# Kernel optimization log

Hardware: AMD Instinct MI355X
Metric: run time of the kernel (lower is better)

The kernel has to match this reference:

```python
import jax, jax.numpy as jnp
import numpy as np

ALPHA = 2.0  # spikingjelly default ATan surrogate alpha
EPS = 1e-5   # BatchNorm eps

@jax.custom_vjp
def heaviside_atan(x):
    return (x >= 0.0).astype(x.dtype)

def _ha_fwd(x):
    return heaviside_atan(x), x

def _ha_bwd(x, g):
    return (g * ALPHA / (2.0 * (1.0 + (jnp.pi / 2.0 * ALPHA * x) ** 2)),)

heaviside_atan.defvjp(_ha_fwd, _ha_bwd)

def lif(x_seq, tau=2.0, v_th=1.0):
    # MultiStepLIFNode, v_reset=0 (hard reset), detach_reset=True
    def step(v, x):
        v = v + (x - v) / tau
        s = heaviside_atan(v - v_th)
        v = v * (1.0 - jax.lax.stop_gradient(s))
        return v, s
    _, spikes = jax.lax.scan(step, jnp.zeros_like(x_seq[0]), x_seq)
    return spikes

def conv_bn(y, Wt, g, b):
    # 1x1 conv (no bias) + BatchNorm2d in training mode over flattened (T*B, H, W)
    y = jnp.einsum('tbchw,oc->tbohw', y, Wt)
    m = y.mean(axis=(0, 1, 3, 4), keepdims=True)
    v = y.var(axis=(0, 1, 3, 4), keepdims=True)
    C = Wt.shape[0]
    return (y - m) / jnp.sqrt(v + EPS) * g.reshape(1, 1, C, 1, 1) + b.reshape(1, 1, C, 1, 1)

def setup_inputs() -> dict:
    key = jax.random.key(0)
    ks = jax.random.split(key, 5)
    T, B, C, H, W = 4, 64, 384, 14, 14
    x = jax.random.normal(ks[0], (T, B, C, H, W), dtype=jnp.float32)
    Wq = jax.random.normal(ks[1], (C, C), dtype=jnp.float32) * 0.02
    Wk = jax.random.normal(ks[2], (C, C), dtype=jnp.float32) * 0.02
    Wv = jax.random.normal(ks[3], (C, C), dtype=jnp.float32) * 0.02
    Wp = jax.random.normal(ks[4], (C, C), dtype=jnp.float32) * 0.02
    ones = jnp.ones((C,), jnp.float32)
    zeros = jnp.zeros((C,), jnp.float32)
    return {"x": x, "Wq": Wq, "Wk": Wk, "Wv": Wv, "Wp": Wp,
            "gq": ones, "bq": zeros, "gk": ones, "bk": zeros,
            "gv": ones, "bv": zeros, "gp": ones, "bp": zeros}

def reference(x, Wq, Wk, Wv, Wp, gq, bq, gk, bk, gv, bv, gp, bp):
    T, B, C, H, W = x.shape
    nh = 8
    dh = C // nh
    N = H * W

    xs = lif(x)  # pre_lif

    def heads(y):  # [T,B,C,H,W] -> [T,B,h,N,dh]
        y = y.reshape(T, B, C, N).transpose(0, 1, 3, 2)
        return y.reshape(T, B, N, nh, dh).transpose(0, 1, 3, 2, 4)

    q = heads(lif(conv_bn(xs, Wq, gq, bq)))
    k = heads(lif(conv_bn(xs, Wk, gk, bk)))
    v = heads(lif(conv_bn(xs, Wv, gv, bv)))

    attn = jnp.einsum('tbhnd,tbhmd->tbhnm', q, k)      # no softmax
    o = jnp.einsum('tbhnm,tbhmd->tbhnd', attn, v) * 0.125
    o = o.transpose(0, 1, 2, 4, 3).reshape(T, B, C, N).reshape(T, B, C, H, W)
    o = lif(o, v_th=0.5)                                # attn_lif
    return conv_bn(o, Wp, gp, bp)                       # proj (no lif)
```

## Files before the change

### kernel.cpp

```cpp
#include <hip/hip_runtime.h>
#include <hip/hip_bf16.h>
#include <stdint.h>

#define T_  4
#define B_  64
#define C_  384
#define N_  196
#define NH  8
#define DH  48
#define TB_ (T_*B_)
#define R_  (T_*B_*N_)
#define NW  12
#define P_  12544
#define NCH 66
#define KG_ 17

typedef float f32x2 __attribute__((ext_vector_type(2)));

__global__ void transpose_w4(const float* __restrict__ s0, const float* __restrict__ s1,
                             const float* __restrict__ s2, const float* __restrict__ s3,
                             float* __restrict__ dst){
    int m = blockIdx.y;
    const float* src = (m==0)?s0:(m==1)?s1:(m==2)?s2:s3;
    int idx = blockIdx.x*256 + threadIdx.x;
    if (idx >= C_*C_) return;
    int o = idx % C_, c = idx / C_;
    dst[(size_t)m*C_*C_ + idx] = src[o*C_ + c];
}

__global__ __launch_bounds__(256) void pre_lif(const float* __restrict__ x,
                                               uint32_t* __restrict__ maskXS){
    int b = blockIdx.x / NW;
    int w = blockIdx.x % NW;
    int n = threadIdx.x;
    if (n >= N_) return;
    float v[32];
#pragma unroll
    for (int j=0;j<32;j++) v[j] = 0.f;
#pragma unroll
    for (int t=0;t<T_;t++){
        uint32_t word = 0;
#pragma unroll
        for (int j=0;j<32;j++){
            int c = w*32 + j;
            float xv = x[((size_t)(t*B_+b)*C_ + c)*N_ + n];
            v[j] = v[j] + (xv - v[j])*0.5f;
            if (v[j] >= 1.0f){ word |= (1u<<j); v[j] = 0.f; }
        }
        maskXS[((size_t)(t*B_+b)*N_ + n)*NW + w] = word;
    }
}

__global__ __launch_bounds__(256) void bit_transpose(const uint32_t* __restrict__ mask,
                                                     unsigned long long* __restrict__ maskT){
    int gw = blockIdx.x*4 + (threadIdx.x>>6);
    int lane = threadIdx.x & 63;
    int kc = gw/12, kw = gw%12;
    uint32_t mwv[12];
#pragma unroll
    for (int w=0;w<12;w++) mwv[w]=0u;
    if (gw < 784){
        int pix = gw*64 + lane;
        const uint4* m4 = (const uint4*)(mask + (size_t)pix*NW);
        uint4 a=m4[0], b=m4[1], c=m4[2];
        mwv[0]=a.x; mwv[1]=a.y; mwv[2]=a.z; mwv[3]=a.w;
        mwv[4]=b.x; mwv[5]=b.y; mwv[6]=b.z; mwv[7]=b.w;
        mwv[8]=c.x; mwv[9]=c.y; mwv[10]=c.z; mwv[11]=c.w;
    }
#pragma unroll
    for (int w=0; w<12; w++){
        uint32_t word = mwv[w];
#pragma unroll
        for (int j=0; j<32; j++){
            unsigned long long bal = __ballot((int)((word>>j)&1u));
            if (lane == 0)
                maskT[((size_t)kc*C_ + (w*32+j))*12 + kw] = bal;
        }
    }
}

__global__ __launch_bounds__(256) void gram(const unsigned long long* __restrict__ maskT,
                                            unsigned int* __restrict__ Gpart){
    __shared__ unsigned int tile[64][49];
    int tid = threadIdx.x, wave = tid>>6, lane = tid&63;
    int kg = blockIdx.x, rg = blockIdx.y, cg = blockIdx.z;
    for (int i=tid; i<64*49; i+=256) ((unsigned int*)tile)[i] = 0u;
    __syncthreads();
    int kc = kg*4 + wave;
    if (kc < NCH){
        const uint4* rp = (const uint4*)(maskT + ((size_t)kc*C_ + rg*64 + lane)*12);
        uint32_t row[24];
#pragma unroll
        for (int q=0;q<6;q++){
            uint4 a = rp[q];
            row[4*q]=a.x; row[4*q+1]=a.y; row[4*q+2]=a.z; row[4*q+3]=a.w;
        }
        for (int cc=0; cc<48; cc++){
            const uint4* cp = (const uint4*)(maskT + ((size_t)kc*C_ + cg*48 + cc)*12);
            uint32_t col[24];
#pragma unroll
            for (int q=0;q<6;q++){
                uint4 a = cp[q];
                col[4*q]=a.x; col[4*q+1]=a.y; col[4*q+2]=a.z; col[4*q+3]=a.w;
            }
            unsigned int s = 0;
#pragma unroll
            for (int q=0;q<24;q++) s += (unsigned int)__popc(row[q]&col[q]);
            atomicAdd(&tile[lane][cc], s);
        }
    }
    __syncthreads();
    unsigned int* out = Gpart + (size_t)kg*C_*C_;
    for (int i=tid; i<64*48; i+=256){
        int r = i/48, cc = i%48;
        out[(size_t)(rg*64+r)*C_ + cg*48 + cc] = tile[r][cc];
    }
}

__global__ __launch_bounds__(256) void gram_reduce(const unsigned int* __restrict__ Gpart,
                                                   float* __restrict__ Gf){
    int e = blockIdx.x*256 + threadIdx.x;
    unsigned int s = 0;
#pragma unroll
    for (int k=0;k<KG_;k++) s += Gpart[(size_t)k*C_*C_ + e];
    Gf[e] = (float)s;
}

__global__ __launch_bounds__(384) void bn_from_gram(const float* __restrict__ Gf,
        const float* __restrict__ WTall,
        const float* __restrict__ g0, const float* __restrict__ b0,
        const float* __restrict__ g1, const float* __restrict__ b1,
        const float* __restrict__ g2, const float* __restrict__ b2,
        float* __restrict__ scaleOut, float* __restrict__ shiftOut, int wtBase){
    __shared__ float w4[384][4];
    __shared__ float sred[8][6];
    int t = threadIdx.x, wave = t>>6, lane = t&63;
    int br = blockIdx.y;
    const float* WT = WTall + (size_t)(wtBase+br)*C_*C_;
    int o0 = blockIdx.x*4;
    float4 wv = *(const float4*)(WT + (size_t)t*C_ + o0);
    w4[t][0]=wv.x; w4[t][1]=wv.y; w4[t][2]=wv.z; w4[t][3]=wv.w;
    __syncthreads();
    float h0=0.f,h1=0.f,h2=0.f,h3=0.f;
#pragma unroll 4
    for (int c=0;c<C_;c++){
        float gv = Gf[(size_t)c*C_ + t];
        float4 wc = *(const float4*)&w4[c][0];
        h0 += gv*wc.x; h1 += gv*wc.y; h2 += gv*wc.z; h3 += gv*wc.w;
    }
    float cnt = Gf[(size_t)t*C_ + t];
    float p0=wv.x*h0, p1=wv.y*h1, p2=wv.z*h2, p3=wv.w*h3;
    float q0=cnt*wv.x, q1=cnt*wv.y, q2=cnt*wv.z, q3=cnt*wv.w;
#pragma unroll
    for (int off=32; off>0; off>>=1){
        p0+=__shfl_down(p0,off); p1+=__shfl_down(p1,off);
        p2+=__shfl_down(p2,off); p3+=__shfl_down(p3,off);
        q0+=__shfl_down(q0,off); q1+=__shfl_down(q1,off);
        q2+=__shfl_down(q2,off); q3+=__shfl_down(q3,off);
    }
    if (lane == 0){
        sred[0][wave]=p0; sred[1][wave]=p1; sred[2][wave]=p2; sred[3][wave]=p3;
        sred[4][wave]=q0; sred[5][wave]=q1; sred[6][wave]=q2; sred[7][wave]=q3;
    }
    __syncthreads();
    if (t < 4){
        const float* g  = (br==0)?g0:(br==1)?g1:g2;
        const float* bb = (br==0)?b0:(br==1)?b1:b2;
        float ss = ((sred[t][0]+sred[t][1])+(sred[t][2]+sred[t][3]))+(sred[t][4]+sred[t][5]);
        float sm = ((sred[4+t][0]+sred[4+t][1])+(sred[4+t][2]+sred[4+t][3]))+(sred[4+t][4]+sred[4+t][5]);
        float m   = sm / (float)R_;
        float var = ss / (float)R_ - m*m;
        float sc  = g[o0+t] / sqrtf(var + 1e-5f);
        scaleOut[br*C_ + o0+t] = sc;
        shiftOut[br*C_ + o0+t] = bb[o0+t] - m*sc;
    }
}

__global__ __launch_bounds__(256) void conv_lif3(const uint32_t* __restrict__ mask,
        const float* __restrict__ WTall,
        const float* __restrict__ scaleAll, const float* __restrict__ shiftAll,
        uint32_t* __restrict__ moQ, uint32_t* __restrict__ moK, uint32_t* __restrict__ moV){
    __shared__ uint16_t lst[4][416];
    __shared__ float scLDS[3*C_];
    __shared__ float shLDS[3*C_];
    int tid = threadIdx.x, wave = tid>>6, lane = tid&63;
    int pix0 = blockIdx.x*4 + wave;
    for (int i=tid; i<3*C_; i+=256){ scLDS[i]=scaleAll[i]; shLDS[i]=shiftAll[i]; }
    __syncthreads();

    float v0[6]={0,0,0,0,0,0}, v1[6]={0,0,0,0,0,0}, v2[6]={0,0,0,0,0,0};
    for (int t=0;t<T_;t++){
        size_t pix = (size_t)t*P_ + pix0;
        const uint4* m4 = (const uint4*)(mask + pix*NW);
        uint4 ma = m4[0], mb = m4[1], mc = m4[2];
        uint32_t mwv[12] = {ma.x,ma.y,ma.z,ma.w, mb.x,mb.y,mb.z,mb.w, mc.x,mc.y,mc.z,mc.w};
        int cnt = 0;
#pragma unroll
        for (int w=0;w<12;w++) cnt += __popc(mwv[w]);
        if (lane < 12){
            int off = 0;
            uint32_t mybits = 0;
#pragma unroll
            for (int w=0;w<12;w++){
                if (w < lane) off += __popc(mwv[w]);
                if (w == lane) mybits = mwv[w];
            }
            while (mybits){
                lst[wave][off++] = (uint16_t)((lane<<5) + __builtin_ctz(mybits));
                mybits &= mybits - 1;
            }
        }
        __syncthreads();

#pragma unroll
        for (int br=0; br<3; ++br){
            const float* WT = WTall + (size_t)br*C_*C_ + lane;
            float ya[6]={0,0,0,0,0,0}, yb[6]={0,0,0,0,0,0};
            float yc[6]={0,0,0,0,0,0}, yd[6]={0,0,0,0,0,0};
            int i = 0;
            for (; i+3 < cnt; i += 4){
                ushort4 cs = *(const ushort4*)&lst[wave][i];
                const float* q0 = WT + (size_t)cs.x*C_;
                const float* q1 = WT + (size_t)cs.y*C_;
                const float* q2 = WT + (size_t)cs.z*C_;
                const float* q3 = WT + (size_t)cs.w*C_;
#pragma unroll
                for (int j=0;j<6;j++){
                    ya[j] += q0[j<<6]; yb[j] += q1[j<<6];
                    yc[j] += q2[j<<6]; yd[j] += q3[j<<6];
                }
            }
            for (; i < cnt; ++i){
                int c = lst[wave][i];
                const float* q0 = WT + (size_t)c*C_;
#pragma unroll
                for (int j=0;j<6;j++) ya[j] += q0[j<<6];
            }
            float* vs = (br==0)?v0:(br==1)?v1:v2;
            uint32_t words[12];
#pragma unroll
            for (int j=0;j<6;j++){
                int o = (j<<6) + lane;
                float val = ((ya[j]+yb[j])+(yc[j]+yd[j]))*scLDS[br*C_+o] + shLDS[br*C_+o];
                float vv = vs[j];
                vv = vv + (val - vv)*0.5f;
                int s = (vv >= 1.0f);
                unsigned long long bal = __ballot(s);
                if (s) vv = 0.f;
                vs[j] = vv;
                words[2*j]   = (uint32_t)bal;
                words[2*j+1] = (uint32_t)(bal>>32);
            }
            if (lane == 0){
                uint32_t* mo = (br==0)?moQ:(br==1)?moK:moV;
                uint4* o4 = (uint4*)(mo + pix*NW);
                o4[0] = make_uint4(words[0],words[1],words[2],words[3]);
                o4[1] = make_uint4(words[4],words[5],words[6],words[7]);
                o4[2] = make_uint4(words[8],words[9],words[10],words[11]);
            }
        }
        __syncthreads();
    }
}

__global__ __launch_bounds__(256) void attention_lif(const uint32_t* __restrict__ mq,
                                                     const uint32_t* __restrict__ mk,
                                                     const uint32_t* __restrict__ mv,
                                                     uint16_t* __restrict__ mo){
    __shared__ unsigned long long kT[DH][4];
    __shared__ unsigned long long vT[DH][4];
    __shared__ uint32_t Cp[DH*25];

    int h = blockIdx.x & 7;
    int b = blockIdx.x >> 3;
    int tid = threadIdx.x, wv = tid>>6, lane = tid&63;
    int sw  = (h*DH) >> 5;
    int shf = (h*DH) & 31;

    float vm[DH];
#pragma unroll
    for (int d=0;d<DH;d++) vm[d] = 0.f;

    for (int t=0;t<T_;t++){
        int tb = t*B_ + b;
        unsigned long long q = 0, kk = 0, vvv = 0;
        if (tid < N_){
            const uint32_t* pq = mq + ((size_t)tb*N_ + tid)*NW + sw;
            const uint32_t* pk = mk + ((size_t)tb*N_ + tid)*NW + sw;
            const uint32_t* pv = mv + ((size_t)tb*N_ + tid)*NW + sw;
            unsigned long long lo, hi;
            lo = pq[0]; hi = pq[1];
            q   = (shf ? ((lo>>16) | (hi<<16)) : (lo | (hi<<32))) & 0xFFFFFFFFFFFFULL;
            lo = pk[0]; hi = pk[1];
            kk  = (shf ? ((lo>>16) | (hi<<16)) : (lo | (hi<<32))) & 0xFFFFFFFFFFFFULL;
            lo = pv[0]; hi = pv[1];
            vvv = (shf ? ((lo>>16) | (hi<<16)) : (lo | (hi<<32))) & 0xFFFFFFFFFFFFULL;
        }
#pragma unroll 1
        for (int d=0; d<DH; d++){
            unsigned long long bk_ = __ballot((int)((kk >>d)&1ull));
            unsigned long long bv_ = __ballot((int)((vvv>>d)&1ull));
            if (lane == 0){ kT[d][wv] = bk_; vT[d][wv] = bv_; }
        }
        __syncthreads();

        if (tid < 240){
            int j  = tid / 5;
            int dg = tid % 5;
            int d0 = dg*10;
            int d1 = (dg==4) ? 48 : d0+10;
            unsigned long long ka=kT[j][0], kb=kT[j][1], kc=kT[j][2], kd=kT[j][3];
            for (int d=d0; d<d1; d+=2){
                uint32_t c0 = (uint32_t)(__popcll(ka&vT[d][0]) + __popcll(kb&vT[d][1])
                            + __popcll(kc&vT[d][2]) + __popcll(kd&vT[d][3]));
                uint32_t c1 = (uint32_t)(__popcll(ka&vT[d+1][0]) + __popcll(kb&vT[d+1][1])
                            + __popcll(kc&vT[d+1][2]) + __popcll(kd&vT[d+1][3]));
                Cp[j*25 + (d>>1)] = c0 | (c1<<16);
            }
        }
        __syncthreads();

        if (tid < N_){
            uint32_t acc[24];
#pragma unroll
            for (int p=0;p<24;p++) acc[p] = 0u;
            unsigned long long qb = q;
            while (qb){
                int j = __builtin_ctzll(qb); qb &= qb-1;
                const uint32_t* row = &Cp[j*25];
#pragma unroll
                for (int p=0;p<24;p++) acc[p] += row[p];
            }
            unsigned long long sp = 0;
#pragma unroll
            for (int d=0; d<DH; d++){
                uint32_t a = (d&1) ? (acc[d>>1]>>16) : (acc[d>>1]&0xFFFFu);
                float o = 0.125f*(float)a;
                vm[d] = vm[d] + (o - vm[d])*0.5f;
                if (vm[d] >= 0.5f){ sp |= (1ull<<d); vm[d] = 0.f; }
            }
            size_t rec = ((size_t)tb*N_ + tid)*24 + 3*h;
            mo[rec]   = (uint16_t)(sp);
            mo[rec+1] = (uint16_t)(sp >> 16);
            mo[rec+2] = (uint16_t)(sp >> 32);
        }
        __syncthreads();
    }
}

__global__ __launch_bounds__(256) void proj_out(const uint32_t* __restrict__ mask,
                                                const float* __restrict__ WT,
                                                const float* __restrict__ scale,
                                                const float* __restrict__ shift,
                                                float* __restrict__ out){
    __shared__ float tile[192][98];
    __shared__ uint16_t lst[4][400];
    int bid = blockIdx.x;
    int tb = bid>>2, nh = (bid>>1)&1, ch = bid&1;
    int n0 = nh*98, c0 = ch*192;
    int tid = threadIdx.x, wave = tid>>6, lane = tid&63;
    float sc[3], sh[3];
#pragma unroll
    for (int i=0;i<3;i++){
        sc[i] = scale[c0+(i<<6)+lane];
        sh[i] = shift[c0+(i<<6)+lane];
    }
    for (int p=wave; p<98; p+=4){
        size_t pix = (size_t)tb*N_ + n0 + p;
        const uint4* m4 = (const uint4*)(mask + pix*NW);
        uint4 ma = m4[0], mb = m4[1], mc = m4[2];
        uint32_t mwv[12] = {ma.x,ma.y,ma.z,ma.w, mb.x,mb.y,mb.z,mb.w, mc.x,mc.y,mc.z,mc.w};
        int cnt = 0;
#pragma unroll
        for (int w=0;w<12;w++) cnt += __popc(mwv[w]);
        if (lane == 0){
            int k = 0;
#pragma unroll
            for (int w=0;w<12;w++){
                uint32_t bits = mwv[w];
                while (bits){
                    lst[wave][k++] = (uint16_t)((w<<5) + __builtin_ctz(bits));
                    bits &= bits - 1;
                }
            }
        }
        float ya[3]={0,0,0}, yb[3]={0,0,0}, yc[3]={0,0,0}, yd[3]={0,0,0};
        int i = 0;
        for (; i+3 < cnt; i += 4){
            ushort4 cs = *(const ushort4*)&lst[wave][i];
            const float* q0 = WT + (size_t)cs.x*C_ + c0 + lane;
            const float* q1 = WT + (size_t)cs.y*C_ + c0 + lane;
            const float* q2 = WT + (size_t)cs.z*C_ + c0 + lane;
            const float* q3 = WT + (size_t)cs.w*C_ + c0 + lane;
#pragma unroll
            for (int j=0;j<3;j++){
                ya[j] += q0[j<<6]; yb[j] += q1[j<<6];
                yc[j] += q2[j<<6]; yd[j] += q3[j<<6];
            }
        }
        for (; i < cnt; ++i){
            int c = lst[wave][i];
            const float* q0 = WT + (size_t)c*C_ + c0 + lane;
#pragma unroll
            for (int j=0;j<3;j++) ya[j] += q0[j<<6];
        }
#pragma unroll
        for (int j=0;j<3;j++)
            tile[(j<<6)+lane][p] = ((ya[j]+yb[j])+(yc[j]+yd[j]))*sc[j] + sh[j];
    }
    __syncthreads();
    for (int r=wave; r<192; r+=4){
        if (lane < 49){
            f32x2 tv = *(const f32x2*)&tile[r][2*lane];
            *(f32x2*)(out + ((size_t)tb*C_ + c0 + r)*N_ + n0 + 2*lane) = tv;
        }
    }
}

extern "C" void kernel_launch(void* const* d_in, const int* in_sizes, int n_in,
                              void* d_out, int out_size, void* d_ws, size_t ws_size,
                              hipStream_t stream) {
    const float* x  = (const float*)d_in[0];
    const float* Wq = (const float*)d_in[1];
    const float* Wk = (const float*)d_in[2];
    const float* Wv = (const float*)d_in[3];
    const float* Wp = (const float*)d_in[4];
    const float* gq = (const float*)d_in[5];
    const float* bq = (const float*)d_in[6];
    const float* gk = (const float*)d_in[7];
    const float* bk = (const float*)d_in[8];
    const float* gv = (const float*)d_in[9];
    const float* bv = (const float*)d_in[10];
    const float* gp = (const float*)d_in[11];
    const float* bp = (const float*)d_in[12];

    char* w = (char*)d_ws;
    size_t off = 0;
    uint32_t* maskXS = (uint32_t*)(w + off); off += (size_t)R_*NW*4;
    uint32_t* maskQ  = (uint32_t*)(w + off); off += (size_t)R_*NW*4;
    uint32_t* maskK  = (uint32_t*)(w + off); off += (size_t)R_*NW*4;
    uint32_t* maskV  = (uint32_t*)(w + off); off += (size_t)R_*NW*4;
    float* WTall = (float*)(w + off); off += (size_t)4*C_*C_*4;
    unsigned long long* maskT = (unsigned long long*)(w + off); off += (size_t)NCH*C_*12*8;
    unsigned int* Gpart = (unsigned int*)(w + off); off += (size_t)KG_*C_*C_*4;
    float* Gf = (float*)(w + off); off += (size_t)C_*C_*4;
    float* scaleB = (float*)(w + off); off += (size_t)4*C_*4;
    float* shiftB = (float*)(w + off); off += (size_t)4*C_*4;
    uint32_t* maskOL = maskXS;

    transpose_w4<<<dim3((C_*C_+255)/256, 4),256,0,stream>>>(Wq, Wk, Wv, Wp, WTall);

    pre_lif<<<B_*NW,256,0,stream>>>(x, maskXS);

    bit_transpose<<<198,256,0,stream>>>(maskXS, maskT);
    gram<<<dim3(KG_,6,8),256,0,stream>>>(maskT, Gpart);
    gram_reduce<<<576,256,0,stream>>>(Gpart, Gf);
    bn_from_gram<<<dim3(96,3),384,0,stream>>>(Gf, WTall, gq,bq, gk,bk, gv,bv,
                                              scaleB, shiftB, 0);

    conv_lif3<<<P_/4,256,0,stream>>>(maskXS, WTall, scaleB, shiftB,
                                     maskQ, maskK, maskV);

    attention_lif<<<B_*NH,256,0,stream>>>(maskQ, maskK, maskV, (uint16_t*)maskOL);

    bit_transpose<<<198,256,0,stream>>>(maskOL, maskT);
    gram<<<dim3(KG_,6,8),256,0,stream>>>(maskT, Gpart);
    gram_reduce<<<576,256,0,stream>>>(Gpart, Gf);
    bn_from_gram<<<dim3(96,1),384,0,stream>>>(Gf, WTall, gp,bp, gp,bp, gp,bp,
                                              scaleB + 3*C_, shiftB + 3*C_, 3);

    proj_out<<<TB_*4,256,0,stream>>>(maskOL, WTall + (size_t)3*C_*C_,
                                     scaleB + 3*C_, shiftB + 3*C_, (float*)d_out);
}
```

Baseline: 418.9 us.

## Fuse gram partial reduction via atomics, split proj_out finer, parallelize index list build

The gram kernel now accumulates its per-block tile straight into a single zeroed counter matrix with global atomics. This removes the 17-slice partial buffer and the separate gram_reduce kernel, at the cost of a memset and atomic contention. proj_out is split into 8 blocks per (t,b) instead of 4, each covering 49 pixels, to raise parallelism. Its sparse-channel list is now built by 12 lanes in parallel using prefix popcounts instead of a serial loop on lane 0. The output store goes from paired float2 writes to scalar writes.

```diff
diff --git a/kernel.cpp b/kernel.cpp
--- a/kernel.cpp
+++ b/kernel.cpp
@@ -80,7 +80,7 @@
 }
 
 __global__ __launch_bounds__(256) void gram(const unsigned long long* __restrict__ maskT,
-                                            unsigned int* __restrict__ Gpart){
+                                            unsigned int* __restrict__ Gu){
     __shared__ unsigned int tile[64][49];
     int tid = threadIdx.x, wave = tid>>6, lane = tid&63;
     int kg = blockIdx.x, rg = blockIdx.y, cg = blockIdx.z;
@@ -110,23 +110,14 @@
         }
     }
     __syncthreads();
-    unsigned int* out = Gpart + (size_t)kg*C_*C_;
     for (int i=tid; i<64*48; i+=256){
         int r = i/48, cc = i%48;
-        out[(size_t)(rg*64+r)*C_ + cg*48 + cc] = tile[r][cc];
-    }
-}
-
-__global__ __launch_bounds__(256) void gram_reduce(const unsigned int* __restrict__ Gpart,
-                                                   float* __restrict__ Gf){
-    int e = blockIdx.x*256 + threadIdx.x;
-    unsigned int s = 0;
-#pragma unroll
-    for (int k=0;k<KG_;k++) s += Gpart[(size_t)k*C_*C_ + e];
-    Gf[e] = (float)s;
-}
-
-__global__ __launch_bounds__(384) void bn_from_gram(const float* __restrict__ Gf,
+        unsigned int v = tile[r][cc];
+        if (v) atomicAdd(&Gu[(size_t)(rg*64+r)*C_ + cg*48 + cc], v);
+    }
+}
+
+__global__ __launch_bounds__(384) void bn_from_gram(const unsigned int* __restrict__ Gu,
         const float* __restrict__ WTall,
         const float* __restrict__ g0, const float* __restrict__ b0,
         const float* __restrict__ g1, const float* __restrict__ b1,
@@ -144,11 +135,11 @@
     float h0=0.f,h1=0.f,h2=0.f,h3=0.f;
 #pragma unroll 4
     for (int c=0;c<C_;c++){
-        float gv = Gf[(size_t)c*C_ + t];
+        float gv = (float)Gu[(size_t)c*C_ + t];
         float4 wc = *(const float4*)&w4[c][0];
         h0 += gv*wc.x; h1 += gv*wc.y; h2 += gv*wc.z; h3 += gv*wc.w;
     }
-    float cnt = Gf[(size_t)t*C_ + t];
+    float cnt = (float)Gu[(size_t)t*C_ + t];
     float p0=wv.x*h0, p1=wv.y*h1, p2=wv.z*h2, p3=wv.w*h3;
     float q0=cnt*wv.x, q1=cnt*wv.y, q2=cnt*wv.z, q3=cnt*wv.w;
 #pragma unroll
@@ -353,11 +344,11 @@
                                                 const float* __restrict__ scale,
                                                 const float* __restrict__ shift,
                                                 float* __restrict__ out){
-    __shared__ float tile[192][98];
-    __shared__ uint16_t lst[4][400];
+    __shared__ float tile[192][49];
+    __shared__ uint16_t lst[4][392];
     int bid = blockIdx.x;
-    int tb = bid>>2, nh = (bid>>1)&1, ch = bid&1;
-    int n0 = nh*98, c0 = ch*192;
+    int tb = bid>>3, r7 = bid&7, nq = r7>>1, ch = r7&1;
+    int n0 = nq*49, c0 = ch*192;
     int tid = threadIdx.x, wave = tid>>6, lane = tid&63;
     float sc[3], sh[3];
 #pragma unroll
@@ -365,7 +356,7 @@
         sc[i] = scale[c0+(i<<6)+lane];
         sh[i] = shift[c0+(i<<6)+lane];
     }
-    for (int p=wave; p<98; p+=4){
+    for (int p=wave; p<49; p+=4){
         size_t pix = (size_t)tb*N_ + n0 + p;
         const uint4* m4 = (const uint4*)(mask + pix*NW);
         uint4 ma = m4[0], mb = m4[1], mc = m4[2];
@@ -373,15 +364,17 @@
         int cnt = 0;
 #pragma unroll
         for (int w=0;w<12;w++) cnt += __popc(mwv[w]);
-        if (lane == 0){
-            int k = 0;
+        if (lane < 12){
+            int off = 0;
+            uint32_t mybits = 0;
 #pragma unroll
             for (int w=0;w<12;w++){
-                uint32_t bits = mwv[w];
-                while (bits){
-                    lst[wave][k++] = (uint16_t)((w<<5) + __builtin_ctz(bits));
-                    bits &= bits - 1;
-                }
+                if (w < lane) off += __popc(mwv[w]);
+                if (w == lane) mybits = mwv[w];
+            }
+            while (mybits){
+                lst[wave][off++] = (uint16_t)((lane<<5) + __builtin_ctz(mybits));
+                mybits &= mybits - 1;
             }
         }
         float ya[3]={0,0,0}, yb[3]={0,0,0}, yc[3]={0,0,0}, yd[3]={0,0,0};
@@ -410,10 +403,8 @@
     }
     __syncthreads();
     for (int r=wave; r<192; r+=4){
-        if (lane < 49){
-            f32x2 tv = *(const f32x2*)&tile[r][2*lane];
-            *(f32x2*)(out + ((size_t)tb*C_ + c0 + r)*N_ + n0 + 2*lane) = tv;
-        }
+        if (lane < 49)
+            out[((size_t)tb*C_ + c0 + r)*N_ + n0 + lane] = tile[r][lane];
     }
 }
 
@@ -442,8 +433,7 @@
     uint32_t* maskV  = (uint32_t*)(w + off); off += (size_t)R_*NW*4;
     float* WTall = (float*)(w + off); off += (size_t)4*C_*C_*4;
     unsigned long long* maskT = (unsigned long long*)(w + off); off += (size_t)NCH*C_*12*8;
-    unsigned int* Gpart = (unsigned int*)(w + off); off += (size_t)KG_*C_*C_*4;
-    float* Gf = (float*)(w + off); off += (size_t)C_*C_*4;
+    unsigned int* Gu = (unsigned int*)(w + off); off += (size_t)C_*C_*4;
     float* scaleB = (float*)(w + off); off += (size_t)4*C_*4;
     float* shiftB = (float*)(w + off); off += (size_t)4*C_*4;
     uint32_t* maskOL = maskXS;
@@ -452,10 +442,10 @@
 
     pre_lif<<<B_*NW,256,0,stream>>>(x, maskXS);
 
+    hipMemsetAsync(Gu, 0, (size_t)C_*C_*4, stream);
     bit_transpose<<<198,256,0,stream>>>(maskXS, maskT);
-    gram<<<dim3(KG_,6,8),256,0,stream>>>(maskT, Gpart);
-    gram_reduce<<<576,256,0,stream>>>(Gpart, Gf);
-    bn_from_gram<<<dim3(96,3),384,0,stream>>>(Gf, WTall, gq,bq, gk,bk, gv,bv,
+    gram<<<dim3(KG_,6,8),256,0,stream>>>(maskT, Gu);
+    bn_from_gram<<<dim3(96,3),384,0,stream>>>(Gu, WTall, gq,bq, gk,bk, gv,bv,
                                               scaleB, shiftB, 0);
 
     conv_lif3<<<P_/4,256,0,stream>>>(maskXS, WTall, scaleB, shiftB,
@@ -463,12 +453,12 @@
 
     attention_lif<<<B_*NH,256,0,stream>>>(maskQ, maskK, maskV, (uint16_t*)maskOL);
 
+    hipMemsetAsync(Gu, 0, (size_t)C_*C_*4, stream);
     bit_transpose<<<198,256,0,stream>>>(maskOL, maskT);
-    gram<<<dim3(KG_,6,8),256,0,stream>>>(maskT, Gpart);
-    gram_reduce<<<576,256,0,stream>>>(Gpart, Gf);
-    bn_from_gram<<<dim3(96,1),384,0,stream>>>(Gf, WTall, gp,bp, gp,bp, gp,bp,
+    gram<<<dim3(KG_,6,8),256,0,stream>>>(maskT, Gu);
+    bn_from_gram<<<dim3(96,1),384,0,stream>>>(Gu, WTall, gp,bp, gp,bp, gp,bp,
                                               scaleB + 3*C_, shiftB + 3*C_, 3);
 
-    proj_out<<<TB_*4,256,0,stream>>>(maskOL, WTall + (size_t)3*C_*C_,
+    proj_out<<<TB_*8,256,0,stream>>>(maskOL, WTall + (size_t)3*C_*C_,
                                      scaleB + 3*C_, shiftB + 3*C_, (float*)d_out);
 }
```

Measured after the change: 402.9 us. 1.04x faster.
